# Kernel tuning notes

Hardware: AMD Instinct MI355X
Metric: run time of the kernel (lower is better)

## Reference

```python
import jax, jax.numpy as jnp
import numpy as np
from jax import lax

B, C, H, W = 8, 19, 512, 512
LOW_T, HIGH_T = 100.0, 200.0  # cv2.Canny(img, 100, 200)
MAX_HYST_ITERS = 256          # safety cap on hysteresis fixed-point iterations

_KX = jnp.array([[-1., 0., 1.], [-2., 0., 2.], [-1., 0., 1.]], jnp.float32)
_KY = jnp.array([[-1., -2., -1.], [0., 0., 0.], [1., 2., 1.]], jnp.float32)


def _conv3(x, k):
    # x: [B, H+2, W+2] (already padded), k: [3,3] -> [B, H, W]
    return lax.conv_general_dilated(x[:, None], k[None, None], (1, 1), 'VALID')[:, 0]


def _dilate3(s):
    # 8-connected boolean dilation via 3x3 max window
    return lax.reduce_window(s.astype(jnp.int32), 0, lax.max, (1, 3, 3), (1, 1, 1), 'SAME') > 0


def _canny(img):
    # img: [B, H, W] float values in [0, 255]. Returns float32 edge map in {0,1}.
    b, h, w = img.shape
    pad = jnp.pad(img, ((0, 0), (1, 1), (1, 1)), mode='edge')
    gx = _conv3(pad, _KX)
    gy = _conv3(pad, _KY)
    mag = jnp.abs(gx) + jnp.abs(gy)  # cv2 default L1 gradient magnitude
    ang = jnp.degrees(jnp.arctan2(gy, gx)) % 180.0
    mp = jnp.pad(mag, ((0, 0), (1, 1), (1, 1)))
    nb = lambda dy, dx: mp[:, 1 + dy:1 + dy + h, 1 + dx:1 + dx + w]
    # non-maximum suppression along quantized gradient direction
    d0 = (ang < 22.5) | (ang >= 157.5)
    d45 = (ang >= 22.5) & (ang < 67.5)
    d90 = (ang >= 67.5) & (ang < 112.5)
    keep0 = (mag >= nb(0, 1)) & (mag >= nb(0, -1))
    keep45 = (mag >= nb(-1, 1)) & (mag >= nb(1, -1))
    keep90 = (mag >= nb(1, 0)) & (mag >= nb(-1, 0))
    keep135 = (mag >= nb(-1, -1)) & (mag >= nb(1, 1))
    keep = jnp.where(d0, keep0, jnp.where(d45, keep45, jnp.where(d90, keep90, keep135)))
    strong = keep & (mag > HIGH_T)
    weak = keep & (mag > LOW_T)  # weak includes strong
    # hysteresis: propagate strong labels through weak pixels to fixed point
    def cond(c):
        s, changed, it = c
        return changed & (it < MAX_HYST_ITERS)
    def body(c):
        s, _, it = c
        s2 = (weak & _dilate3(s)) | strong
        return (s2, jnp.any(s2 != s), it + 1)
    edges, _, _ = lax.while_loop(cond, body, (strong, jnp.array(True), jnp.array(0)))
    return edges.astype(jnp.float32)


def setup_inputs() -> dict:
    key = jax.random.key(0)
    k1, k2 = jax.random.split(key)
    pred = jax.random.normal(k1, (B, C, H, W), dtype=jnp.float32)
    labels = jax.random.uniform(k2, (B, H, W), dtype=jnp.float32)
    return {'pred': pred, 'labels': labels}


def reference(pred, labels):
    # pred_convert: per-pixel argmax over channel dim -> class ids [B, H, W]
    cls = jnp.argmax(pred, axis=1)
    # canny(): (img * 255).astype('uint8') -- class ids wrap mod 256
    img_p = ((cls * 255) % 256).astype(jnp.float32)
    # labels in [0,1): uint8 cast truncates toward zero
    img_l = jnp.floor(labels * 255.0)
    ep = _canny(img_p)  # [B, H, W] in {0,1}
    el = _canny(img_l)  # [B, H, W] in {0,1}
    # nn.CrossEntropyLoss() on float target of same shape: input [N=B, C=H, d1=W],
    # target is class probabilities; mean over N and d1.
    logp = jax.nn.log_softmax(ep, axis=1)
    return jnp.mean(jnp.sum(-el * logp, axis=1))
```

## Files before the change

kernel.cpp:

```cpp
#include <hip/hip_runtime.h>
#include <hip/hip_bf16.h>
#include <math.h>

typedef unsigned long long u64;
typedef unsigned char u8;
typedef unsigned short u16;
typedef unsigned int u32;

#define BB 8
#define CC 19
#define HH 512
#define WW 512
#define HWSZ (HH*WW)
#define NIMG 16

__global__ __launch_bounds__(256) void k_argmax(const float* __restrict__ pred,
                                                u8* __restrict__ img) {
    int idx = blockIdx.x * 256 + threadIdx.x;
    int p4 = idx * 4;
    int b = p4 / HWSZ;
    int rem = p4 - b * HWSZ;
    const float4* base = (const float4*)(pred + (size_t)b * CC * HWSZ + rem);
    float4 best = base[0];
    int ix = 0, iy = 0, iz = 0, iw = 0;
    for (int c = 1; c < CC; ++c) {
        float4 v = base[(size_t)c * (HWSZ / 4)];
        if (v.x > best.x) { best.x = v.x; ix = c; }
        if (v.y > best.y) { best.y = v.y; iy = c; }
        if (v.z > best.z) { best.z = v.z; iz = c; }
        if (v.w > best.w) { best.w = v.w; iw = c; }
    }
    uchar4 o;
    o.x = (u8)(-ix); o.y = (u8)(-iy); o.z = (u8)(-iz); o.w = (u8)(-iw);
    *(uchar4*)(img + p4) = o;
}

__global__ __launch_bounds__(256) void k_imgl(const float* __restrict__ lab,
                                              u8* __restrict__ img) {
    int idx = blockIdx.x * 256 + threadIdx.x;
    int p4 = idx * 4;
    float4 v = *(const float4*)(lab + p4);
    uchar4 o;
    o.x = (u8)(v.x * 255.0f);
    o.y = (u8)(v.y * 255.0f);
    o.z = (u8)(v.z * 255.0f);
    o.w = (u8)(v.w * 255.0f);
    *(uchar4*)(img + p4) = o;
}

__global__ __launch_bounds__(256) void k_grad(const u8* __restrict__ imgs,
                                              u16* __restrict__ magdir) {
    int t = blockIdx.x * 256 + threadIdx.x;
    int x0 = (t & 63) * 8;
    int y  = (t >> 6) & 511;
    int im = t >> 15;
    const u8* base = imgs + (size_t)im * HWSZ;
    int rows[3];
    rows[0] = (y == 0) ? 0 : y - 1;
    rows[1] = y;
    rows[2] = (y == 511) ? 511 : y + 1;
    int bb[3][10];
#pragma unroll
    for (int r = 0; r < 3; ++r) {
        const u8* rp = base + rows[r] * WW;
        u64 m = *(const u64*)(rp + x0);
        bb[r][0] = (x0 == 0) ? rp[0] : rp[x0 - 1];
#pragma unroll
        for (int i = 0; i < 8; ++i) bb[r][i + 1] = (int)((m >> (8 * i)) & 0xFF);
        bb[r][9] = (x0 == 504) ? rp[511] : rp[x0 + 8];
    }
    u32 v[8];
#pragma unroll
    for (int i = 0; i < 8; ++i) {
        int a00 = bb[0][i], a01 = bb[0][i + 1], a02 = bb[0][i + 2];
        int a10 = bb[1][i],                     a12 = bb[1][i + 2];
        int a20 = bb[2][i], a21 = bb[2][i + 1], a22 = bb[2][i + 2];
        int gx = (a02 + 2 * a12 + a22) - (a00 + 2 * a10 + a20);
        int gy = (a20 + 2 * a21 + a22) - (a00 + 2 * a01 + a02);
        int ax = gx < 0 ? -gx : gx;
        int ay = gy < 0 ? -gy : gy;
        int mag = ax + ay;
        float fax = (float)ax, fay = (float)ay;
        int dir;
        if (fay < 0.41421356237309515f * fax) dir = 0;
        else if (fay >= 2.414213562373095f * fax) dir = 2;
        else dir = ((gx ^ gy) >= 0) ? 1 : 3;
        v[i] = (u32)mag | ((u32)dir << 12);
    }
    uint4 o;
    o.x = v[0] | (v[1] << 16);
    o.y = v[2] | (v[3] << 16);
    o.z = v[4] | (v[5] << 16);
    o.w = v[6] | (v[7] << 16);
    *(uint4*)(magdir + (size_t)im * HWSZ + y * WW + x0) = o;
}

__global__ __launch_bounds__(256) void k_nms(const u16* __restrict__ magdir,
                                             u64* __restrict__ weak,
                                             u64* __restrict__ strong) {
    int t = blockIdx.x * 256 + threadIdx.x;
    int x  = t & 511;
    int y  = (t >> 9) & 511;
    int im = t >> 18;
    const u16* md = magdir + (size_t)im * HWSZ;
    u32 v = md[y * WW + x];
    int mag = v & 0xFFF;
    int dir = v >> 12;
    auto M = [&](int yy, int xx) -> int {
        if ((unsigned)yy > 511u || (unsigned)xx > 511u) return 0;
        return md[yy * WW + xx] & 0xFFF;
    };
    int n1, n2;
    switch (dir) {
        case 0:  n1 = M(y, x - 1);     n2 = M(y, x + 1);     break;
        case 1:  n1 = M(y - 1, x + 1); n2 = M(y + 1, x - 1); break;
        case 2:  n1 = M(y - 1, x);     n2 = M(y + 1, x);     break;
        default: n1 = M(y - 1, x - 1); n2 = M(y + 1, x + 1); break;
    }
    bool keep = (mag >= n1) && (mag >= n2);
    u64 wb = __ballot(keep && mag > 100);
    u64 sb = __ballot(keep && mag > 200);
    if ((threadIdx.x & 63) == 0) {
        size_t w = ((size_t)im * HH + y) * 8 + (x >> 6);
        weak[w] = wb;
        strong[w] = sb;
    }
}

__global__ __launch_bounds__(512) void k_hyst(const u64* __restrict__ weakg,
                                              const u64* __restrict__ strongg,
                                              u64* __restrict__ edges) {
    __shared__ u64 h[512][8];
    __shared__ int flags[2];
    int y = threadIdx.x;
    int im = blockIdx.x;
    size_t base = ((size_t)im * HH + y) * 8;
    u64 wk[8], st[8], s[8];
#pragma unroll
    for (int j = 0; j < 8; ++j) {
        wk[j] = weakg[base + j];
        st[j] = strongg[base + j];
        s[j] = st[j];
    }
    for (int it = 0; it < 256; ++it) {
        u64 hh[8];
#pragma unroll
        for (int j = 0; j < 8; ++j) hh[j] = s[j] | (s[j] << 1) | (s[j] >> 1);
#pragma unroll
        for (int j = 1; j < 8; ++j) hh[j] |= s[j - 1] >> 63;
#pragma unroll
        for (int j = 0; j < 7; ++j) hh[j] |= s[j + 1] << 63;
#pragma unroll
        for (int j = 0; j < 8; ++j) h[y][j] = hh[j];
        if (threadIdx.x == 0 && it == 0) flags[0] = 0;
        __syncthreads();
        if (threadIdx.x == 0) flags[(it + 1) & 1] = 0;
        int changed = 0;
#pragma unroll
        for (int j = 0; j < 8; ++j) {
            u64 up = (y > 0)   ? h[y - 1][j] : 0ull;
            u64 dn = (y < 511) ? h[y + 1][j] : 0ull;
            u64 ns = (wk[j] & (hh[j] | up | dn)) | st[j];
            changed |= (ns != s[j]);
            s[j] = ns;
        }
        if (changed) flags[it & 1] = 1;
        __syncthreads();
        if (!flags[it & 1]) break;
    }
#pragma unroll
    for (int j = 0; j < 8; ++j) edges[base + j] = s[j];
}

__global__ void k_zero(float* out) {
    if (threadIdx.x == 0 && blockIdx.x == 0) out[0] = 0.0f;
}

__global__ __launch_bounds__(256) void k_loss(const u64* __restrict__ edges,
                                              float* __restrict__ out) {
    int b = blockIdx.x >> 3;
    int j = blockIdx.x & 7;
    int wave = threadIdx.x >> 6;
    int lane = threadIdx.x & 63;
    const u64* ep = edges + ((size_t)b * HH) * 8 + j;
    const u64* el = edges + ((size_t)(b + 8) * HH) * 8 + j;
    int k = 0, es = 0, ov = 0;
    int y0 = wave * 128;
    for (int y = y0; y < y0 + 128; ++y) {
        u64 wp = ep[(size_t)y * 8];
        u64 wl = el[(size_t)y * 8];
        int bp = (int)((wp >> lane) & 1ull);
        int bl = (int)((wl >> lane) & 1ull);
        k += bp; es += bl; ov += (bp & bl);
    }
    __shared__ int red[3][4][64];
    red[0][wave][lane] = k;
    red[1][wave][lane] = es;
    red[2][wave][lane] = ov;
    __syncthreads();
    if (threadIdx.x < 64) {
        int l = threadIdx.x;
        int K = red[0][0][l] + red[0][1][l] + red[0][2][l] + red[0][3][l];
        int E = red[1][0][l] + red[1][1][l] + red[1][2][l] + red[1][3][l];
        int O = red[2][0][l] + red[2][1][l] + red[2][2][l] + red[2][3][l];
        float logZ = logf(512.0f + 1.7182818284590452f * (float)K);
        float v = ((float)E * logZ - (float)O) * (1.0f / 4096.0f);
#pragma unroll
        for (int o = 32; o > 0; o >>= 1) v += __shfl_down(v, o, 64);
        if (l == 0) atomicAdd(out, v);
    }
}

extern "C" void kernel_launch(void* const* d_in, const int* in_sizes, int n_in,
                              void* d_out, int out_size, void* d_ws, size_t ws_size,
                              hipStream_t stream) {
    const float* pred = (const float*)d_in[0];
    const float* labels = (const float*)d_in[1];
    float* out = (float*)d_out;

    u8*  imgs   = (u8*)d_ws;
    u16* magdir = (u16*)((char*)d_ws + (size_t)NIMG * HWSZ);
    u64* weak   = (u64*)((char*)d_ws + (size_t)NIMG * HWSZ * 3);
    u64* strong = (u64*)((char*)weak + (size_t)NIMG * HH * 8 * 8);
    u64* edges  = (u64*)((char*)strong + (size_t)NIMG * HH * 8 * 8);

    hipLaunchKernelGGL(k_argmax, dim3(BB * HWSZ / 4 / 256), dim3(256), 0, stream,
                       pred, imgs);
    hipLaunchKernelGGL(k_imgl, dim3(BB * HWSZ / 4 / 256), dim3(256), 0, stream,
                       labels, imgs + (size_t)BB * HWSZ);
    hipLaunchKernelGGL(k_grad, dim3(NIMG * HH * 64 / 256), dim3(256), 0, stream,
                       imgs, magdir);
    hipLaunchKernelGGL(k_nms, dim3(NIMG * HWSZ / 256), dim3(256), 0, stream,
                       magdir, weak, strong);
    hipLaunchKernelGGL(k_hyst, dim3(NIMG), dim3(512), 0, stream,
                       weak, strong, edges);
    hipLaunchKernelGGL(k_zero, dim3(1), dim3(64), 0, stream, out);
    hipLaunchKernelGGL(k_loss, dim3(64), dim3(256), 0, stream, edges, out);
}
```

Measured before the change: 272.0 us.

## Pre-propagate hysteresis in parallel 64x64 tiles before global fixed-point pass

Adds a tile-local hysteresis kernel where each wavefront owns a 64x64 tile and iterates to a local fixed point using shuffles and a ballot-based exit, reading halo rows and columns from the current edge map. Three passes run before the single-block-per-image global hysteresis kernel, which now starts from the pre-propagated edges instead of the strong map. The goal is to use many CUs for most of the propagation so the 16-block global kernel needs fewer block-wide synchronised iterations. The cost is extra launches and memory traffic, and the tile kernels race on neighbouring tiles' edge words, which is tolerated because the result is monotone and the global pass fixes any remainder.

```diff
diff --git a/kernel.cpp b/kernel.cpp
--- a/kernel.cpp
+++ b/kernel.cpp
@@ -97,7 +97,8 @@
 
 __global__ __launch_bounds__(256) void k_nms(const u16* __restrict__ magdir,
                                              u64* __restrict__ weak,
-                                             u64* __restrict__ strong) {
+                                             u64* __restrict__ strong,
+                                             u64* __restrict__ edges) {
     int t = blockIdx.x * 256 + threadIdx.x;
     int x  = t & 511;
     int y  = (t >> 9) & 511;
@@ -124,7 +125,49 @@
         size_t w = ((size_t)im * HH + y) * 8 + (x >> 6);
         weak[w] = wb;
         strong[w] = sb;
-    }
+        edges[w] = sb;
+    }
+}
+
+__global__ __launch_bounds__(256) void k_hyst_tile(const u64* __restrict__ weakg,
+                                                   u64* __restrict__ edges) {
+    int wv = blockIdx.x * 4 + (threadIdx.x >> 6);
+    int lane = threadIdx.x & 63;
+    int im = wv >> 6;
+    int ty = (wv >> 3) & 7;
+    int tx = wv & 7;
+    int row = ty * 64 + lane;
+    size_t base = (size_t)im * (HH * 8) + (size_t)row * 8 + tx;
+    u64 s  = edges[base];
+    u64 wk = weakg[base];
+    u64 wl = (tx > 0) ? edges[base - 1] : 0ull;
+    u64 wr = (tx < 7) ? edges[base + 1] : 0ull;
+    u64 lb = wl >> 63;
+    u64 rb = (wr & 1ull) << 63;
+    u64 up_h = 0ull, dn_h = 0ull;
+    if (lane == 0 && ty > 0) {
+        u64 uw = edges[base - 8];
+        u64 ul = (tx > 0) ? edges[base - 9] : 0ull;
+        u64 ur = (tx < 7) ? edges[base - 7] : 0ull;
+        up_h = uw | (uw << 1) | (uw >> 1) | (ul >> 63) | ((ur & 1ull) << 63);
+    }
+    if (lane == 63 && ty < 7) {
+        u64 dw = edges[base + 8];
+        u64 dl = (tx > 0) ? edges[base + 7] : 0ull;
+        u64 dr = (tx < 7) ? edges[base + 9] : 0ull;
+        dn_h = dw | (dw << 1) | (dw >> 1) | (dl >> 63) | ((dr & 1ull) << 63);
+    }
+    for (int it = 0; it < 130; ++it) {
+        u64 hh = s | (s << 1) | (s >> 1) | lb | rb;
+        u64 up = __shfl_up(hh, 1);
+        if (lane == 0) up = up_h;
+        u64 dn = __shfl_down(hh, 1);
+        if (lane == 63) dn = dn_h;
+        u64 t = wk & (hh | up | dn) & ~s;
+        if (__ballot(t != 0ull) == 0ull) break;
+        s |= t;
+    }
+    edges[base] = s;
 }
 
 __global__ __launch_bounds__(512) void k_hyst(const u64* __restrict__ weakg,
@@ -140,7 +183,7 @@
     for (int j = 0; j < 8; ++j) {
         wk[j] = weakg[base + j];
         st[j] = strongg[base + j];
-        s[j] = st[j];
+        s[j] = edges[base + j];
     }
     for (int it = 0; it < 256; ++it) {
         u64 hh[8];
@@ -160,7 +203,7 @@
         for (int j = 0; j < 8; ++j) {
             u64 up = (y > 0)   ? h[y - 1][j] : 0ull;
             u64 dn = (y < 511) ? h[y + 1][j] : 0ull;
-            u64 ns = (wk[j] & (hh[j] | up | dn)) | st[j];
+            u64 ns = (wk[j] & (hh[j] | up | dn)) | st[j] | s[j];
             changed |= (ns != s[j]);
             s[j] = ns;
         }
@@ -231,7 +274,10 @@
     hipLaunchKernelGGL(k_grad, dim3(NIMG * HH * 64 / 256), dim3(256), 0, stream,
                        imgs, magdir);
     hipLaunchKernelGGL(k_nms, dim3(NIMG * HWSZ / 256), dim3(256), 0, stream,
-                       magdir, weak, strong);
+                       magdir, weak, strong, edges);
+    hipLaunchKernelGGL(k_hyst_tile, dim3(256), dim3(256), 0, stream, weak, edges);
+    hipLaunchKernelGGL(k_hyst_tile, dim3(256), dim3(256), 0, stream, weak, edges);
+    hipLaunchKernelGGL(k_hyst_tile, dim3(256), dim3(256), 0, stream, weak, edges);
     hipLaunchKernelGGL(k_hyst, dim3(NIMG), dim3(512), 0, stream,
                        weak, strong, edges);
     hipLaunchKernelGGL(k_zero, dim3(1), dim3(64), 0, stream, out);
```

After: 282.3 us. 3.8% more time.

## Propagate hysteresis along rows with carry-add trick, split shared layout, fuse prep kernels

Applied to the files above, without the earlier changes.

The hysteresis loop now runs a full horizontal flood fill of strong bits through weak runs in each row in every iteration. It uses the add-with-carry trick forward across the 8 words and again in bit-reversed order backward. This should cut the number of block-synchronised iterations, since long horizontal edges no longer advance one pixel per iteration. The shared buffer is split into lo/hi u32 arrays laid out column-major, which may reduce LDS bank conflicts. The argmax, label-quantise and zero-init kernels are merged into one launch. The cost is extra ALU work and bit reversals per iteration.

```diff
diff --git a/kernel.cpp b/kernel.cpp
--- a/kernel.cpp
+++ b/kernel.cpp
@@ -14,9 +14,12 @@
 #define HWSZ (HH*WW)
 #define NIMG 16
 
-__global__ __launch_bounds__(256) void k_argmax(const float* __restrict__ pred,
-                                                u8* __restrict__ img) {
+__global__ __launch_bounds__(256) void k_pre(const float* __restrict__ pred,
+                                             const float* __restrict__ lab,
+                                             u8* __restrict__ img,
+                                             float* __restrict__ out) {
     int idx = blockIdx.x * 256 + threadIdx.x;
+    if (idx == 0) out[0] = 0.0f;
     int p4 = idx * 4;
     int b = p4 / HWSZ;
     int rem = p4 - b * HWSZ;
@@ -33,19 +36,13 @@
     uchar4 o;
     o.x = (u8)(-ix); o.y = (u8)(-iy); o.z = (u8)(-iz); o.w = (u8)(-iw);
     *(uchar4*)(img + p4) = o;
-}
-
-__global__ __launch_bounds__(256) void k_imgl(const float* __restrict__ lab,
-                                              u8* __restrict__ img) {
-    int idx = blockIdx.x * 256 + threadIdx.x;
-    int p4 = idx * 4;
     float4 v = *(const float4*)(lab + p4);
-    uchar4 o;
-    o.x = (u8)(v.x * 255.0f);
-    o.y = (u8)(v.y * 255.0f);
-    o.z = (u8)(v.z * 255.0f);
-    o.w = (u8)(v.w * 255.0f);
-    *(uchar4*)(img + p4) = o;
+    uchar4 ol;
+    ol.x = (u8)(v.x * 255.0f);
+    ol.y = (u8)(v.y * 255.0f);
+    ol.z = (u8)(v.z * 255.0f);
+    ol.w = (u8)(v.w * 255.0f);
+    *(uchar4*)(img + (size_t)BB * HWSZ + p4) = ol;
 }
 
 __global__ __launch_bounds__(256) void k_grad(const u8* __restrict__ imgs,
@@ -130,19 +127,44 @@
 __global__ __launch_bounds__(512) void k_hyst(const u64* __restrict__ weakg,
                                               const u64* __restrict__ strongg,
                                               u64* __restrict__ edges) {
-    __shared__ u64 h[512][8];
+    __shared__ u32 hlo[8][512];
+    __shared__ u32 hhi[8][512];
     __shared__ int flags[2];
     int y = threadIdx.x;
     int im = blockIdx.x;
     size_t base = ((size_t)im * HH + y) * 8;
-    u64 wk[8], st[8], s[8];
+    u64 wk[8], s[8];
 #pragma unroll
     for (int j = 0; j < 8; ++j) {
         wk[j] = weakg[base + j];
-        st[j] = strongg[base + j];
-        s[j] = st[j];
+        s[j] = strongg[base + j];
     }
     for (int it = 0; it < 256; ++it) {
+        u64 diff = 0;
+        u64 c = 0;
+#pragma unroll
+        for (int j = 0; j < 8; ++j) {
+            u64 a = s[j], w = wk[j];
+            u64 t1 = a + w;       u64 c1 = (u64)(t1 < a);
+            u64 t2 = t1 + c;      u64 c2 = (u64)(t2 < t1);
+            u64 ns = a | ((t2 ^ w) & w);
+            diff |= ns ^ a;
+            s[j] = ns;
+            c = c1 | c2;
+        }
+        c = 0;
+#pragma unroll
+        for (int j = 7; j >= 0; --j) {
+            u64 a = __builtin_bitreverse64(s[j]);
+            u64 w = __builtin_bitreverse64(wk[j]);
+            u64 t1 = a + w;       u64 c1 = (u64)(t1 < a);
+            u64 t2 = t1 + c;      u64 c2 = (u64)(t2 < t1);
+            u64 nsr = a | ((t2 ^ w) & w);
+            u64 ns = __builtin_bitreverse64(nsr);
+            diff |= ns ^ s[j];
+            s[j] = ns;
+            c = c1 | c2;
+        }
         u64 hh[8];
 #pragma unroll
         for (int j = 0; j < 8; ++j) hh[j] = s[j] | (s[j] << 1) | (s[j] >> 1);
@@ -151,29 +173,27 @@
 #pragma unroll
         for (int j = 0; j < 7; ++j) hh[j] |= s[j + 1] << 63;
 #pragma unroll
-        for (int j = 0; j < 8; ++j) h[y][j] = hh[j];
-        if (threadIdx.x == 0 && it == 0) flags[0] = 0;
+        for (int j = 0; j < 8; ++j) {
+            hlo[j][y] = (u32)hh[j];
+            hhi[j][y] = (u32)(hh[j] >> 32);
+        }
+        if (y == 0 && it == 0) flags[0] = 0;
         __syncthreads();
-        if (threadIdx.x == 0) flags[(it + 1) & 1] = 0;
-        int changed = 0;
+        if (y == 0) flags[(it + 1) & 1] = 0;
 #pragma unroll
         for (int j = 0; j < 8; ++j) {
-            u64 up = (y > 0)   ? h[y - 1][j] : 0ull;
-            u64 dn = (y < 511) ? h[y + 1][j] : 0ull;
-            u64 ns = (wk[j] & (hh[j] | up | dn)) | st[j];
-            changed |= (ns != s[j]);
-            s[j] = ns;
-        }
-        if (changed) flags[it & 1] = 1;
+            u64 up = (y > 0)   ? ((u64)hlo[j][y - 1] | ((u64)hhi[j][y - 1] << 32)) : 0ull;
+            u64 dn = (y < 511) ? ((u64)hlo[j][y + 1] | ((u64)hhi[j][y + 1] << 32)) : 0ull;
+            u64 t = wk[j] & (up | dn) & ~s[j];
+            diff |= t;
+            s[j] |= t;
+        }
+        if (diff) flags[it & 1] = 1;
         __syncthreads();
         if (!flags[it & 1]) break;
     }
 #pragma unroll
     for (int j = 0; j < 8; ++j) edges[base + j] = s[j];
-}
-
-__global__ void k_zero(float* out) {
-    if (threadIdx.x == 0 && blockIdx.x == 0) out[0] = 0.0f;
 }
 
 __global__ __launch_bounds__(256) void k_loss(const u64* __restrict__ edges,
@@ -224,16 +244,13 @@
     u64* strong = (u64*)((char*)weak + (size_t)NIMG * HH * 8 * 8);
     u64* edges  = (u64*)((char*)strong + (size_t)NIMG * HH * 8 * 8);
 
-    hipLaunchKernelGGL(k_argmax, dim3(BB * HWSZ / 4 / 256), dim3(256), 0, stream,
-                       pred, imgs);
-    hipLaunchKernelGGL(k_imgl, dim3(BB * HWSZ / 4 / 256), dim3(256), 0, stream,
-                       labels, imgs + (size_t)BB * HWSZ);
+    hipLaunchKernelGGL(k_pre, dim3(BB * HWSZ / 4 / 256), dim3(256), 0, stream,
+                       pred, labels, imgs, out);
     hipLaunchKernelGGL(k_grad, dim3(NIMG * HH * 64 / 256), dim3(256), 0, stream,
                        imgs, magdir);
     hipLaunchKernelGGL(k_nms, dim3(NIMG * HWSZ / 256), dim3(256), 0, stream,
                        magdir, weak, strong);
     hipLaunchKernelGGL(k_hyst, dim3(NIMG), dim3(512), 0, stream,
                        weak, strong, edges);
-    hipLaunchKernelGGL(k_zero, dim3(1), dim3(64), 0, stream, out);
     hipLaunchKernelGGL(k_loss, dim3(64), dim3(256), 0, stream, edges, out);
 }
```

After: 270.6 us. Within noise of the previous version (-0.5%).
